# Kernel tuning notes

Measured on AMD Instinct MI355X. Metric: run time of the kernel, lower is better.

The kernel has to match this reference:

```python
import jax, jax.numpy as jnp
import numpy as np

S, B, N, K, D, H = 4, 8, 2048, 16, 32, 128


def setup_inputs() -> dict:
    key = jax.random.key(0)
    ks = jax.random.split(key, 7)
    x = jax.random.normal(ks[0], (S, B, N, D), dtype=jnp.float32)
    mu = jax.random.normal(ks[1], (S, B, K, D), dtype=jnp.float32)
    tau = jax.random.uniform(ks[2], (S, B, K, D), dtype=jnp.float32)  # precisions > 0
    # Linear(3D -> H); stored as (3D, H) i.e. transpose of torch's (H, 3D) weight
    W1 = jax.random.normal(ks[3], (3 * D, H), dtype=jnp.float32) * (1.0 / np.sqrt(3 * D))
    b1 = jax.random.normal(ks[4], (H,), dtype=jnp.float32) * 0.01
    W2 = jax.random.normal(ks[5], (H, 1), dtype=jnp.float32) * (1.0 / np.sqrt(H))
    b2 = jax.random.normal(ks[6], (1,), dtype=jnp.float32) * 0.01
    return {"x": x, "mu": mu, "tau": tau, "W1": W1, "b1": b1, "W2": W2, "b2": b2}


def reference(x, mu, tau, W1, b1, W2, b2):
    # Original torch code materializes var = cat([x_expand, mu_expand, tau_expand], -1)
    # of shape (S,B,N,K,3D) then applies Linear(3D,H). Mathematically identical:
    # split W1 rows into the x / mu / tau blocks and add the partial projections,
    # which avoids building the (S,B,N,K,3D) concat tensor.
    d = x.shape[-1]
    Wx, Wm, Wt = W1[:d], W1[d:2 * d], W1[2 * d:]
    hx = jnp.einsum('sbnd,dh->sbnh', x, Wx)                       # (S,B,N,H)
    hk = jnp.einsum('sbkd,dh->sbkh', mu, Wm) \
       + jnp.einsum('sbkd,dh->sbkh', tau, Wt)                     # (S,B,K,H)
    h = jnp.tanh(hx[:, :, :, None, :] + hk[:, :, None, :, :] + b1)  # (S,B,N,K,H)
    gamma = jnp.einsum('sbnkh,h->sbnk', h, W2[:, 0]) + b2[0]        # (S,B,N,K)
    q_probs = jax.nn.softmax(gamma, axis=-1)
    return q_probs
```

## Files before the change

### kernel.cpp

```cpp
#include <hip/hip_runtime.h>
#include <math.h>

typedef _Float16 half_t;
typedef __attribute__((ext_vector_type(8))) _Float16 half8;

#define EXP2F(x) __builtin_amdgcn_exp2f(x)
#define RCPF(x)  __builtin_amdgcn_rcpf(x)
#define C_SCALE 2.8853900817779268f

__global__ __launch_bounds__(256) void prep_kernel(
    const float* __restrict__ mu, const float* __restrict__ tau,
    const float* __restrict__ W1, const float* __restrict__ b1,
    const float* __restrict__ W2,
    half_t* __restrict__ ek, half_t* __restrict__ w2h) {
  int g = blockIdx.x * 256 + threadIdx.x;
  int h = g & 127, row = g >> 7;
  const float* mur  = mu  + row * 32;
  const float* taur = tau + row * 32;
  float acc = b1[h];
#pragma unroll
  for (int d = 0; d < 32; ++d) {
    acc = fmaf(mur[d],  W1[(32 + d) * 128 + h], acc);
    acc = fmaf(taur[d], W1[(64 + d) * 128 + h], acc);
  }
  ek[g] = (half_t)EXP2F(C_SCALE * acc);
  if (g < 128) w2h[g] = (half_t)(-2.0f * W2[g]);
}

__global__ __launch_bounds__(256, 3) void main_kernel(
    const float* __restrict__ x, const float* __restrict__ W1,
    const half_t* __restrict__ ek, const half_t* __restrict__ w2h,
    float* __restrict__ out) {
  __shared__ __align__(16) float  sX[64][36];
  __shared__ __align__(16) float  sW[32][132];
  __shared__ __align__(16) half_t sEx[64][136];
  __shared__ __align__(16) half_t sEk[16][136];
  __shared__ __align__(16) half_t sW2[128];

  int t = threadIdx.x;
  int row0 = blockIdx.x * 64;
  int sb = row0 >> 11;

  const float4* x4 = (const float4*)(x + (size_t)row0 * 32);
#pragma unroll
  for (int i = 0; i < 2; ++i) {
    int j = i * 256 + t;
    int n = j >> 3, d4 = j & 7;
    *(float4*)&sX[n][d4 * 4] = x4[j];
  }
  const float4* w4 = (const float4*)W1;
#pragma unroll
  for (int i = 0; i < 4; ++i) {
    int j = i * 256 + t;
    int d = j >> 5, h4 = j & 31;
    float4 v = w4[j];
    v.x *= C_SCALE; v.y *= C_SCALE; v.z *= C_SCALE; v.w *= C_SCALE;
    *(float4*)&sW[d][h4 * 4] = v;
  }
  {
    const float4* ek4 = (const float4*)(ek + (size_t)sb * 2048);
    int k = t >> 4, h8 = t & 15;
    *(float4*)&sEk[k][h8 * 8] = ek4[t];
  }
  if (t < 16) *(float4*)&sW2[t * 8] = ((const float4*)w2h)[t];
  __syncthreads();

  {
    int hg = t & 15, rg = t >> 4;
    int h0 = hg * 8, r0 = rg * 4;
    float acc[4][8];
#pragma unroll
    for (int j = 0; j < 4; ++j)
#pragma unroll
      for (int l = 0; l < 8; ++l) acc[j][l] = 0.f;
#pragma unroll 4
    for (int d = 0; d < 32; ++d) {
      float4 wa = *(const float4*)&sW[d][h0];
      float4 wb = *(const float4*)&sW[d][h0 + 4];
      float w[8] = {wa.x, wa.y, wa.z, wa.w, wb.x, wb.y, wb.z, wb.w};
#pragma unroll
      for (int j = 0; j < 4; ++j) {
        float xv = sX[r0 + j][d];
#pragma unroll
        for (int l = 0; l < 8; ++l) acc[j][l] = fmaf(xv, w[l], acc[j][l]);
      }
    }
#pragma unroll
    for (int j = 0; j < 4; ++j) {
      half8 hv;
#pragma unroll
      for (int l = 0; l < 8; ++l) hv[l] = (half_t)EXP2F(acc[j][l]);
      *(half8*)&sEx[r0 + j][h0] = hv;
    }
  }
  __syncthreads();

  int kg = t & 7, rg = t >> 3;
  int r0 = rg * 2, k0 = kg * 2;
  float a00 = 0.f, a01 = 0.f, a10 = 0.f, a11 = 0.f;
#pragma unroll 2
  for (int h8 = 0; h8 < 16; ++h8) {
    half8 ex0 = *(const half8*)&sEx[r0][h8 * 8];
    half8 ex1 = *(const half8*)&sEx[r0 + 1][h8 * 8];
    half8 ekv0 = *(const half8*)&sEk[k0][h8 * 8];
    half8 ekv1 = *(const half8*)&sEk[k0 + 1][h8 * 8];
    half8 wv = *(const half8*)&sW2[h8 * 8];
#pragma unroll
    for (int j = 0; j < 8; ++j) {
      float e0 = (float)ex0[j], e1 = (float)ex1[j];
      float f0 = (float)ekv0[j], f1 = (float)ekv1[j];
      float w = (float)wv[j];
      a00 = fmaf(w, RCPF(fmaf(e0, f0, 1.0f)), a00);
      a01 = fmaf(w, RCPF(fmaf(e0, f1, 1.0f)), a01);
      a10 = fmaf(w, RCPF(fmaf(e1, f0, 1.0f)), a10);
      a11 = fmaf(w, RCPF(fmaf(e1, f1, 1.0f)), a11);
    }
  }

  const float l2e = 1.4426950408889634f;
  {
    float m = fmaxf(a00, a01);
#pragma unroll
    for (int s = 1; s < 8; s <<= 1) m = fmaxf(m, __shfl_xor(m, s, 8));
    float p0 = EXP2F((a00 - m) * l2e), p1 = EXP2F((a01 - m) * l2e);
    float sum = p0 + p1;
#pragma unroll
    for (int s = 1; s < 8; s <<= 1) sum += __shfl_xor(sum, s, 8);
    float inv = RCPF(sum);
    float2 o = make_float2(p0 * inv, p1 * inv);
    *(float2*)&out[(size_t)(row0 + r0) * 16 + k0] = o;
  }
  {
    float m = fmaxf(a10, a11);
#pragma unroll
    for (int s = 1; s < 8; s <<= 1) m = fmaxf(m, __shfl_xor(m, s, 8));
    float p0 = EXP2F((a10 - m) * l2e), p1 = EXP2F((a11 - m) * l2e);
    float sum = p0 + p1;
#pragma unroll
    for (int s = 1; s < 8; s <<= 1) sum += __shfl_xor(sum, s, 8);
    float inv = RCPF(sum);
    float2 o = make_float2(p0 * inv, p1 * inv);
    *(float2*)&out[(size_t)(row0 + r0 + 1) * 16 + k0] = o;
  }
}

extern "C" void kernel_launch(void* const* d_in, const int* in_sizes, int n_in,
                              void* d_out, int out_size, void* d_ws, size_t ws_size,
                              hipStream_t stream) {
  const float* x   = (const float*)d_in[0];
  const float* mu  = (const float*)d_in[1];
  const float* tau = (const float*)d_in[2];
  const float* W1  = (const float*)d_in[3];
  const float* b1  = (const float*)d_in[4];
  const float* W2  = (const float*)d_in[5];
  float* out = (float*)d_out;

  half_t* ek  = (half_t*)d_ws;
  half_t* w2h = ek + 512 * 128;
  (void)in_sizes; (void)n_in; (void)out_size; (void)ws_size;

  prep_kernel<<<256, 256, 0, stream>>>(mu, tau, W1, b1, W2, ek, w2h);
  main_kernel<<<1024, 256, 0, stream>>>(x, W1, ek, w2h, out);
}
```

Baseline: 92.36 us.

## Fuse prep kernel into main kernel and read W1 directly from global

```diff
diff --git a/kernel.cpp b/kernel.cpp
--- a/kernel.cpp
+++ b/kernel.cpp
@@ -8,31 +8,12 @@
 #define RCPF(x)  __builtin_amdgcn_rcpf(x)
 #define C_SCALE 2.8853900817779268f
 
-__global__ __launch_bounds__(256) void prep_kernel(
-    const float* __restrict__ mu, const float* __restrict__ tau,
-    const float* __restrict__ W1, const float* __restrict__ b1,
-    const float* __restrict__ W2,
-    half_t* __restrict__ ek, half_t* __restrict__ w2h) {
-  int g = blockIdx.x * 256 + threadIdx.x;
-  int h = g & 127, row = g >> 7;
-  const float* mur  = mu  + row * 32;
-  const float* taur = tau + row * 32;
-  float acc = b1[h];
-#pragma unroll
-  for (int d = 0; d < 32; ++d) {
-    acc = fmaf(mur[d],  W1[(32 + d) * 128 + h], acc);
-    acc = fmaf(taur[d], W1[(64 + d) * 128 + h], acc);
-  }
-  ek[g] = (half_t)EXP2F(C_SCALE * acc);
-  if (g < 128) w2h[g] = (half_t)(-2.0f * W2[g]);
-}
-
-__global__ __launch_bounds__(256, 3) void main_kernel(
-    const float* __restrict__ x, const float* __restrict__ W1,
-    const half_t* __restrict__ ek, const half_t* __restrict__ w2h,
+__global__ __launch_bounds__(256, 4) void fused_kernel(
+    const float* __restrict__ x, const float* __restrict__ mu,
+    const float* __restrict__ tau, const float* __restrict__ W1,
+    const float* __restrict__ b1, const float* __restrict__ W2,
     float* __restrict__ out) {
   __shared__ __align__(16) float  sX[64][36];
-  __shared__ __align__(16) float  sW[32][132];
   __shared__ __align__(16) half_t sEx[64][136];
   __shared__ __align__(16) half_t sEk[16][136];
   __shared__ __align__(16) half_t sW2[128];
@@ -46,23 +27,20 @@
   for (int i = 0; i < 2; ++i) {
     int j = i * 256 + t;
     int n = j >> 3, d4 = j & 7;
-    *(float4*)&sX[n][d4 * 4] = x4[j];
+    float4 v = x4[j];
+    v.x *= C_SCALE; v.y *= C_SCALE; v.z *= C_SCALE; v.w *= C_SCALE;
+    *(float4*)&sX[n][d4 * 4] = v;
   }
-  const float4* w4 = (const float4*)W1;
-#pragma unroll
-  for (int i = 0; i < 4; ++i) {
-    int j = i * 256 + t;
-    int d = j >> 5, h4 = j & 31;
-    float4 v = w4[j];
-    v.x *= C_SCALE; v.y *= C_SCALE; v.z *= C_SCALE; v.w *= C_SCALE;
-    *(float4*)&sW[d][h4 * 4] = v;
+  if (t < 16) {
+    float4 a = ((const float4*)W2)[2 * t];
+    float4 b = ((const float4*)W2)[2 * t + 1];
+    half8 hv;
+    hv[0] = (half_t)(-2.f * a.x); hv[1] = (half_t)(-2.f * a.y);
+    hv[2] = (half_t)(-2.f * a.z); hv[3] = (half_t)(-2.f * a.w);
+    hv[4] = (half_t)(-2.f * b.x); hv[5] = (half_t)(-2.f * b.y);
+    hv[6] = (half_t)(-2.f * b.z); hv[7] = (half_t)(-2.f * b.w);
+    *(half8*)&sW2[t * 8] = hv;
   }
-  {
-    const float4* ek4 = (const float4*)(ek + (size_t)sb * 2048);
-    int k = t >> 4, h8 = t & 15;
-    *(float4*)&sEk[k][h8 * 8] = ek4[t];
-  }
-  if (t < 16) *(float4*)&sW2[t * 8] = ((const float4*)w2h)[t];
   __syncthreads();
 
   {
@@ -73,10 +51,11 @@
     for (int j = 0; j < 4; ++j)
 #pragma unroll
       for (int l = 0; l < 8; ++l) acc[j][l] = 0.f;
+    const float* Wp = W1 + h0;
 #pragma unroll 4
     for (int d = 0; d < 32; ++d) {
-      float4 wa = *(const float4*)&sW[d][h0];
-      float4 wb = *(const float4*)&sW[d][h0 + 4];
+      float4 wa = *(const float4*)(Wp + d * 128);
+      float4 wb = *(const float4*)(Wp + d * 128 + 4);
       float w[8] = {wa.x, wa.y, wa.z, wa.w, wb.x, wb.y, wb.z, wb.w};
 #pragma unroll
       for (int j = 0; j < 4; ++j) {
@@ -92,6 +71,47 @@
       for (int l = 0; l < 8; ++l) hv[l] = (half_t)EXP2F(acc[j][l]);
       *(half8*)&sEx[r0 + j][h0] = hv;
     }
+  }
+
+  {
+    int k = t >> 4, h0 = (t & 15) * 8;
+    const float4* mu4  = (const float4*)(mu  + ((size_t)sb * 16 + k) * 32);
+    const float4* tau4 = (const float4*)(tau + ((size_t)sb * 16 + k) * 32);
+    float acc[8];
+    {
+      float4 ba = *(const float4*)(b1 + h0);
+      float4 bb = *(const float4*)(b1 + h0 + 4);
+      acc[0] = ba.x; acc[1] = ba.y; acc[2] = ba.z; acc[3] = ba.w;
+      acc[4] = bb.x; acc[5] = bb.y; acc[6] = bb.z; acc[7] = bb.w;
+    }
+    const float* Wm = W1 + 32 * 128 + h0;
+    const float* Wt = W1 + 64 * 128 + h0;
+#pragma unroll 2
+    for (int d4 = 0; d4 < 8; ++d4) {
+      float4 m4 = mu4[d4], t4 = tau4[d4];
+      float mv4[4] = {m4.x, m4.y, m4.z, m4.w};
+      float tv4[4] = {t4.x, t4.y, t4.z, t4.w};
+#pragma unroll
+      for (int dd = 0; dd < 4; ++dd) {
+        int d = d4 * 4 + dd;
+        float4 wma = *(const float4*)(Wm + d * 128);
+        float4 wmb = *(const float4*)(Wm + d * 128 + 4);
+        float4 wta = *(const float4*)(Wt + d * 128);
+        float4 wtb = *(const float4*)(Wt + d * 128 + 4);
+        float wm[8] = {wma.x, wma.y, wma.z, wma.w, wmb.x, wmb.y, wmb.z, wmb.w};
+        float wt[8] = {wta.x, wta.y, wta.z, wta.w, wtb.x, wtb.y, wtb.z, wtb.w};
+        float mv = mv4[dd], tv = tv4[dd];
+#pragma unroll
+        for (int l = 0; l < 8; ++l) {
+          acc[l] = fmaf(mv, wm[l], acc[l]);
+          acc[l] = fmaf(tv, wt[l], acc[l]);
+        }
+      }
+    }
+    half8 hv;
+#pragma unroll
+    for (int l = 0; l < 8; ++l) hv[l] = (half_t)EXP2F(C_SCALE * acc[l]);
+    *(half8*)&sEk[k][h0] = hv;
   }
   __syncthreads();
 
@@ -154,11 +174,7 @@
   const float* b1  = (const float*)d_in[4];
   const float* W2  = (const float*)d_in[5];
   float* out = (float*)d_out;
+  (void)in_sizes; (void)n_in; (void)out_size; (void)d_ws; (void)ws_size;
 
-  half_t* ek  = (half_t*)d_ws;
-  half_t* w2h = ek + 512 * 128;
-  (void)in_sizes; (void)n_in; (void)out_size; (void)ws_size;
-
-  prep_kernel<<<256, 256, 0, stream>>>(mu, tau, W1, b1, W2, ek, w2h);
-  main_kernel<<<1024, 256, 0, stream>>>(x, W1, ek, w2h, out);
+  fused_kernel<<<1024, 256, 0, stream>>>(x, mu, tau, W1, b1, W2, out);
 }
```

New measurement: 103.9 us. 12.5% more time.
